# Optimization experiments

Hardware: AMD Instinct MI355X
Metric: run time of the kernel (lower is better)

The kernel has to match this reference:

```python
import jax, jax.numpy as jnp
import numpy as np


def setup_inputs() -> dict:
    key = jax.random.key(0)
    ks = jax.random.split(key, 8)
    B, N, D, E = 8, 64, 64, 32
    nodes = jax.random.normal(ks[0], (B, N, D), dtype=jnp.float32)
    edges = jax.random.normal(ks[1], (B, N * N, E), dtype=jnp.float32)
    mask = jax.random.uniform(ks[2], (B, N * N, 1), dtype=jnp.float32)
    W_e = jax.random.normal(ks[3], (E, D * D), dtype=jnp.float32) * 0.05
    b_e = jnp.zeros((D * D,), dtype=jnp.float32)
    gru_kernel = jax.random.normal(ks[4], (D, 3 * D), dtype=jnp.float32) * 0.05
    gru_rkernel = jax.random.normal(ks[5], (D, 3 * D), dtype=jnp.float32) * 0.05
    gru_bias = jnp.zeros((2, 3 * D), dtype=jnp.float32)
    return {"nodes": nodes, "edges": edges, "mask": mask, "W_e": W_e,
            "b_e": b_e, "gru_kernel": gru_kernel, "gru_rkernel": gru_rkernel,
            "gru_bias": gru_bias}


def _gru_step(x, h, K, R, bias):
    # keras GRU with reset_after=True
    D = h.shape[-1]
    xk = x @ K + bias[0]          # [M, 3D]
    hk = h @ R + bias[1]          # [M, 3D]
    xz, xr, xh = xk[:, :D], xk[:, D:2 * D], xk[:, 2 * D:]
    hz, hr, hh_ = hk[:, :D], hk[:, D:2 * D], hk[:, 2 * D:]
    z = jax.nn.sigmoid(xz + hz)
    r = jax.nn.sigmoid(xr + hr)
    hh = jnp.tanh(xh + r * hh_)
    return z * h + (1.0 - z) * hh


def reference(nodes, edges, mask, W_e, b_e, gru_kernel, gru_rkernel, gru_bias):
    B, N, D = nodes.shape
    # edge-conditioned transform matrices: [B, N*N, D, D]
    A = jax.nn.relu(edges @ W_e + b_e).reshape(B, N * N, D, D)
    # state_j = tile(nodes, [1, N, 1]) -> [B, N*N, D]
    state_j = jnp.tile(nodes, (1, N, 1))
    # per-edge small matmul A @ node_j
    messages = jnp.einsum('beij,bej->bei', A, state_j)  # [B, N*N, D]
    masked = (messages * mask).reshape(B, N, N, D)
    agg = masked.sum(axis=2)  # [B, N, D]
    # GRU over length-2 sequence [old_state, agg_messages], batch B*N, h0=0
    h = jnp.zeros((B * N, D), dtype=nodes.dtype)
    h = _gru_step(nodes.reshape(B * N, D), h, gru_kernel, gru_rkernel, gru_bias)
    h = _gru_step(agg.reshape(B * N, D), h, gru_kernel, gru_rkernel, gru_bias)
    return h.reshape(B, N, D)
```

## Files before the change

### kernel.cpp

```cpp
#include <hip/hip_runtime.h>

typedef _Float16 half8 __attribute__((ext_vector_type(8)));
typedef float floatx4 __attribute__((ext_vector_type(4)));
typedef float floatx2 __attribute__((ext_vector_type(2)));

#define BB 8
#define NN 64
#define DD 64
#define EE 32

__device__ __forceinline__ float sigmoidf_(float x) { return 1.f / (1.f + __expf(-x)); }
__device__ __forceinline__ float tanhf_(float x) {
    float e = __expf(2.f * x);
    return (e - 1.f) / (e + 1.f);
}
__device__ __forceinline__ floatx2 relu2(floatx2 v) {
    floatx2 z = {0.f, 0.f};
    return __builtin_elementwise_max(v, z);
}

__global__ void prep_kernel(const float* __restrict__ W_e,
                            const float* __restrict__ nodes,
                            const float* __restrict__ K,
                            const float* __restrict__ bias,
                            _Float16* __restrict__ WT,
                            float* __restrict__ h1) {
    const int tid = threadIdx.x;
    if (blockIdx.x < 64) {
        const int d  = blockIdx.x * 64 + (tid & 63);
        const int kq = tid >> 6;
        half8 buf;
#pragma unroll
        for (int j = 0; j < 8; ++j)
            buf[j] = (_Float16)W_e[(kq * 8 + j) * 4096 + d];
        *reinterpret_cast<half8*>(WT + d * 32 + kq * 8) = buf;
    } else {
        const int blk = blockIdx.x - 64;
        const int rr  = tid >> 6;
        const int d   = tid & 63;
        const int row = blk * 4 + rr;
        __shared__ float xs[4][64];
        xs[rr][d] = nodes[row * 64 + d];
        __syncthreads();
        float xz = bias[d], xr = bias[64 + d], xh = bias[128 + d];
#pragma unroll 8
        for (int k = 0; k < 64; ++k) {
            float xv = xs[rr][k];
            xz = fmaf(xv, K[k * 192 + d],       xz);
            xr = fmaf(xv, K[k * 192 + 64 + d],  xr);
            xh = fmaf(xv, K[k * 192 + 128 + d], xh);
        }
        float z  = sigmoidf_(xz + bias[192 + d]);
        float r  = sigmoidf_(xr + bias[256 + d]);
        float hh = tanhf_(xh + r * bias[320 + d]);
        h1[row * 64 + d] = (1.f - z) * hh;
    }
}

__global__ __launch_bounds__(512, 4)
void fused_kernel(const _Float16* __restrict__ WT,
                  const float* __restrict__ edges,
                  const float* __restrict__ nodes,
                  const float* __restrict__ mask,
                  const float* __restrict__ b_e,
                  const float* __restrict__ K,
                  const float* __restrict__ R,
                  const float* __restrict__ bias,
                  const float* __restrict__ h1,
                  float* __restrict__ out) {
    const int b     = blockIdx.x >> 6;
    const int inode = blockIdx.x & 63;
    const int tid   = threadIdx.x;
    const int w     = tid >> 6;
    const int jw    = w & 3;
    const int ibase = (w >> 2) * 32;
    const int lane  = tid & 63;
    const int quad  = lane >> 4;
    const int col   = lane & 15;
    const int row   = b * 64 + inode;

    __shared__ float S[64][4][17];
    __shared__ float P[4][64];
    __shared__ float aggs[64], h1s[64];
    __shared__ float g1[192], g2[192];

    if (tid < 64) h1s[tid] = h1[row * 64 + tid];

    half8 ef[4];
#pragma unroll
    for (int eb = 0; eb < 4; ++eb) {
        const float* ep = edges + (b * 4096 + inode * 64 + eb * 16 + col) * 32 + quad * 8;
        floatx4 e0 = *reinterpret_cast<const floatx4*>(ep);
        floatx4 e1 = *reinterpret_cast<const floatx4*>(ep + 4);
#pragma unroll
        for (int j = 0; j < 4; ++j) {
            ef[eb][j]     = (_Float16)e0[j];
            ef[eb][4 + j] = (_Float16)e1[j];
        }
    }

    floatx2 xm[4][2];
#pragma unroll
    for (int eb = 0; eb < 4; ++eb) {
        int j = eb * 16 + col;
        float mk = mask[b * 4096 + inode * 64 + j];
#pragma unroll
        for (int r = 0; r < 4; ++r) {
            int jj = jw * 16 + quad * 4 + r;
            xm[eb][r >> 1][r & 1] = mk * nodes[(b * 64 + j) * 64 + jj];
        }
    }

    const _Float16* aptr = WT + (jw * 16 + col) * 32 + quad * 8;
    const float*    bptr = b_e + jw * 16 + quad * 4;

    half8   af0 = *reinterpret_cast<const half8*>(aptr + ibase * 2048);
    floatx4 bf0 = *reinterpret_cast<const floatx4*>(bptr + ibase * 64);
    half8   af1 = *reinterpret_cast<const half8*>(aptr + (ibase + 1) * 2048);
    floatx4 bf1 = *reinterpret_cast<const floatx4*>(bptr + (ibase + 1) * 64);

    for (int ii = 0; ii < 32; ++ii) {
        int ip2 = ibase + ((ii + 2) & 31);
        half8   afn = *reinterpret_cast<const half8*>(aptr + ip2 * 2048);
        floatx4 bfn = *reinterpret_cast<const floatx4*>(bptr + ip2 * 64);

        floatx4 c[4];
        c[0] = __builtin_amdgcn_mfma_f32_16x16x32_f16(af0, ef[0], bf0, 0, 0, 0);
        c[1] = __builtin_amdgcn_mfma_f32_16x16x32_f16(af0, ef[1], bf0, 0, 0, 0);
        c[2] = __builtin_amdgcn_mfma_f32_16x16x32_f16(af0, ef[2], bf0, 0, 0, 0);
        c[3] = __builtin_amdgcn_mfma_f32_16x16x32_f16(af0, ef[3], bf0, 0, 0, 0);

        floatx2 sv = {0.f, 0.f};
#pragma unroll
        for (int eb = 0; eb < 4; ++eb) {
            floatx2* cp = reinterpret_cast<floatx2*>(&c[eb]);
            sv += relu2(cp[0]) * xm[eb][0];
            sv += relu2(cp[1]) * xm[eb][1];
        }
        float s = sv[0] + sv[1];
        s += __shfl_xor(s, 32);
        s += __shfl_xor(s, 16);
        if (lane < 16) S[ibase + ii][jw][lane] = s;

        af0 = af1; bf0 = bf1; af1 = afn; bf1 = bfn;
    }
    __syncthreads();

    if (tid < 256) {
        int ii = tid & 63, ww = tid >> 6;
        float p = 0.f;
#pragma unroll
        for (int l = 0; l < 16; ++l) p += S[ii][ww][l];
        P[ww][ii] = p;
    }
    __syncthreads();
    if (tid < 64) aggs[tid] = P[0][tid] + P[1][tid] + P[2][tid] + P[3][tid];
    __syncthreads();

    if (tid < 192) {
        float a1 = bias[tid], a2 = bias[192 + tid];
#pragma unroll 8
        for (int k = 0; k < 64; ++k) {
            a1 = fmaf(aggs[k], K[k * 192 + tid], a1);
            a2 = fmaf(h1s[k],  R[k * 192 + tid], a2);
        }
        g1[tid] = a1; g2[tid] = a2;
    }
    __syncthreads();
    if (tid < 64) {
        float z  = sigmoidf_(g1[tid]       + g2[tid]);
        float r  = sigmoidf_(g1[64 + tid]  + g2[64 + tid]);
        float hh = tanhf_  (g1[128 + tid] + r * g2[128 + tid]);
        out[row * 64 + tid] = z * h1s[tid] + (1.f - z) * hh;
    }
}

extern "C" void kernel_launch(void* const* d_in, const int* in_sizes, int n_in,
                              void* d_out, int out_size, void* d_ws, size_t ws_size,
                              hipStream_t stream) {
    const float* nodes = (const float*)d_in[0];
    const float* edges = (const float*)d_in[1];
    const float* mask  = (const float*)d_in[2];
    const float* W_e   = (const float*)d_in[3];
    const float* b_e   = (const float*)d_in[4];
    const float* gk    = (const float*)d_in[5];
    const float* gr    = (const float*)d_in[6];
    const float* gb    = (const float*)d_in[7];
    float* out = (float*)d_out;

    char* ws = (char*)d_ws;
    _Float16* WT = (_Float16*)ws;
    float*    h1 = (float*)(ws + 262144);

    prep_kernel<<<192, 256, 0, stream>>>(W_e, nodes, gk, gb, WT, h1);
    fused_kernel<<<512, 512, 0, stream>>>(WT, edges, nodes, mask, b_e, gk, gr, gb, h1, out);
}
```

Measured before the change: 97.82 us.

## Fuse first GRU step into main kernel and shorten cross-lane reduction

The first GRU step (nodes @ K plus gates) moves out of the prep kernel into the fused kernel. Idle threads compute it while the message-reduction threads run, which removes the h1 workspace round trip and leaves prep with only the W_e transpose. The in-loop butterfly drops from two shuffles to one permlane32 swap, and the LDS scratch is transposed to hold 32 partials per row. The second-step K and R matvecs are also split across separate thread groups so they run in parallel, at the cost of a longer final 32-element sum.

```diff
diff --git a/kernel.cpp b/kernel.cpp
--- a/kernel.cpp
+++ b/kernel.cpp
@@ -3,6 +3,7 @@
 typedef _Float16 half8 __attribute__((ext_vector_type(8)));
 typedef float floatx4 __attribute__((ext_vector_type(4)));
 typedef float floatx2 __attribute__((ext_vector_type(2)));
+typedef unsigned int uintx2 __attribute__((ext_vector_type(2)));
 
 #define BB 8
 #define NN 64
@@ -19,42 +20,15 @@
     return __builtin_elementwise_max(v, z);
 }
 
-__global__ void prep_kernel(const float* __restrict__ W_e,
-                            const float* __restrict__ nodes,
-                            const float* __restrict__ K,
-                            const float* __restrict__ bias,
-                            _Float16* __restrict__ WT,
-                            float* __restrict__ h1) {
+__global__ void prep_kernel(const float* __restrict__ W_e, _Float16* __restrict__ WT) {
     const int tid = threadIdx.x;
-    if (blockIdx.x < 64) {
-        const int d  = blockIdx.x * 64 + (tid & 63);
-        const int kq = tid >> 6;
-        half8 buf;
+    const int d   = blockIdx.x * 64 + (tid & 63);
+    const int kq  = tid >> 6;
+    half8 buf;
 #pragma unroll
-        for (int j = 0; j < 8; ++j)
-            buf[j] = (_Float16)W_e[(kq * 8 + j) * 4096 + d];
-        *reinterpret_cast<half8*>(WT + d * 32 + kq * 8) = buf;
-    } else {
-        const int blk = blockIdx.x - 64;
-        const int rr  = tid >> 6;
-        const int d   = tid & 63;
-        const int row = blk * 4 + rr;
-        __shared__ float xs[4][64];
-        xs[rr][d] = nodes[row * 64 + d];
-        __syncthreads();
-        float xz = bias[d], xr = bias[64 + d], xh = bias[128 + d];
-#pragma unroll 8
-        for (int k = 0; k < 64; ++k) {
-            float xv = xs[rr][k];
-            xz = fmaf(xv, K[k * 192 + d],       xz);
-            xr = fmaf(xv, K[k * 192 + 64 + d],  xr);
-            xh = fmaf(xv, K[k * 192 + 128 + d], xh);
-        }
-        float z  = sigmoidf_(xz + bias[192 + d]);
-        float r  = sigmoidf_(xr + bias[256 + d]);
-        float hh = tanhf_(xh + r * bias[320 + d]);
-        h1[row * 64 + d] = (1.f - z) * hh;
-    }
+    for (int j = 0; j < 8; ++j)
+        buf[j] = (_Float16)W_e[(kq * 8 + j) * 4096 + d];
+    *reinterpret_cast<half8*>(WT + d * 32 + kq * 8) = buf;
 }
 
 __global__ __launch_bounds__(512, 4)
@@ -66,7 +40,6 @@
                   const float* __restrict__ K,
                   const float* __restrict__ R,
                   const float* __restrict__ bias,
-                  const float* __restrict__ h1,
                   float* __restrict__ out) {
     const int b     = blockIdx.x >> 6;
     const int inode = blockIdx.x & 63;
@@ -79,12 +52,12 @@
     const int col   = lane & 15;
     const int row   = b * 64 + inode;
 
-    __shared__ float S[64][4][17];
+    __shared__ float S[4][32][65];
     __shared__ float P[4][64];
-    __shared__ float aggs[64], h1s[64];
-    __shared__ float g1[192], g2[192];
+    __shared__ float aggs[64], h1s[64], ns[64];
+    __shared__ float gx[192], g1[192], g2[192];
 
-    if (tid < 64) h1s[tid] = h1[row * 64 + tid];
+    if (tid < 64) ns[tid] = nodes[row * 64 + tid];
 
     half8 ef[4];
 #pragma unroll
@@ -138,9 +111,15 @@
             sv += relu2(cp[1]) * xm[eb][1];
         }
         float s = sv[0] + sv[1];
+
+#if __has_builtin(__builtin_amdgcn_permlane32_swap)
+        uintx2 pr = __builtin_amdgcn_permlane32_swap(__float_as_uint(s), __float_as_uint(s),
+                                                     false, false);
+        s = __uint_as_float(pr[0]) + __uint_as_float(pr[1]);
+#else
         s += __shfl_xor(s, 32);
-        s += __shfl_xor(s, 16);
-        if (lane < 16) S[ibase + ii][jw][lane] = s;
+#endif
+        if (lane < 32) S[jw][lane][ibase + ii] = s;
 
         af0 = af1; bf0 = bf1; af1 = afn; bf1 = bfn;
     }
@@ -150,27 +129,46 @@
         int ii = tid & 63, ww = tid >> 6;
         float p = 0.f;
 #pragma unroll
-        for (int l = 0; l < 16; ++l) p += S[ii][ww][l];
+        for (int l = 0; l < 32; ++l) p += S[ww][l][ii];
         P[ww][ii] = p;
+    } else if (tid < 448) {
+        int t = tid - 256;
+        float a = bias[t];
+#pragma unroll 8
+        for (int k = 0; k < 64; ++k) a = fmaf(ns[k], K[k * 192 + t], a);
+        gx[t] = a;
     }
     __syncthreads();
-    if (tid < 64) aggs[tid] = P[0][tid] + P[1][tid] + P[2][tid] + P[3][tid];
+
+    if (tid < 64) {
+        aggs[tid] = P[0][tid] + P[1][tid] + P[2][tid] + P[3][tid];
+    } else if (tid < 128) {
+        int d = tid - 64;
+        float z  = sigmoidf_(gx[d]       + bias[192 + d]);
+        float r  = sigmoidf_(gx[64 + d]  + bias[256 + d]);
+        float hh = tanhf_   (gx[128 + d] + r * bias[320 + d]);
+        h1s[d] = (1.f - z) * hh;
+    }
     __syncthreads();
 
     if (tid < 192) {
-        float a1 = bias[tid], a2 = bias[192 + tid];
+        float a1 = bias[tid];
 #pragma unroll 8
-        for (int k = 0; k < 64; ++k) {
-            a1 = fmaf(aggs[k], K[k * 192 + tid], a1);
-            a2 = fmaf(h1s[k],  R[k * 192 + tid], a2);
-        }
-        g1[tid] = a1; g2[tid] = a2;
+        for (int k = 0; k < 64; ++k) a1 = fmaf(aggs[k], K[k * 192 + tid], a1);
+        g1[tid] = a1;
+    } else if (tid < 384) {
+        int t = tid - 192;
+        float a2 = bias[192 + t];
+#pragma unroll 8
+        for (int k = 0; k < 64; ++k) a2 = fmaf(h1s[k], R[k * 192 + t], a2);
+        g2[t] = a2;
     }
     __syncthreads();
+
     if (tid < 64) {
         float z  = sigmoidf_(g1[tid]       + g2[tid]);
         float r  = sigmoidf_(g1[64 + tid]  + g2[64 + tid]);
-        float hh = tanhf_  (g1[128 + tid] + r * g2[128 + tid]);
+        float hh = tanhf_   (g1[128 + tid] + r * g2[128 + tid]);
         out[row * 64 + tid] = z * h1s[tid] + (1.f - z) * hh;
     }
 }
@@ -188,10 +186,8 @@
     const float* gb    = (const float*)d_in[7];
     float* out = (float*)d_out;
 
-    char* ws = (char*)d_ws;
-    _Float16* WT = (_Float16*)ws;
-    float*    h1 = (float*)(ws + 262144);
+    _Float16* WT = (_Float16*)d_ws;
 
-    prep_kernel<<<192, 256, 0, stream>>>(W_e, nodes, gk, gb, WT, h1);
-    fused_kernel<<<512, 512, 0, stream>>>(WT, edges, nodes, mask, b_e, gk, gr, gb, h1, out);
+    prep_kernel<<<64, 256, 0, stream>>>(W_e, WT);
+    fused_kernel<<<512, 512, 0, stream>>>(WT, edges, nodes, mask, b_e, gk, gr, gb, out);
 }
```

New measurement: 94.86 us. -3.0%, faster.
